# Performance work log

Hardware: AMD Instinct MI355X
Metric: run time of the kernel (lower is better)

Reference implementation:

```python
import jax, jax.numpy as jnp
import numpy as np

# Model hyperparameters (match init_kwargs)
B, REF_P, IN_P, OUT_P = 32, 256, 256, 256
K, KS = 4, 3
RATIO = 0.25
HIDDEN = int(REF_P * RATIO) + 1  # 65, per canonical attention1d
TEMP = 34.0
STRIDE, PAD, DIL, GROUPS = 1, 1, 1, 1
L, L_REF = 4096, 64


def setup_inputs() -> dict:
    key = jax.random.key(0)
    k0, k1, k2, k3, k4 = jax.random.split(key, 5)
    ref = jax.random.normal(k0, (B, REF_P, L_REF), dtype=jnp.float32)
    x = jax.random.normal(k1, (B, IN_P, L), dtype=jnp.float32)
    # attention1d params: fc1 (1x1 conv, no bias), fc2 (1x1 conv, with bias)
    att_w1 = jax.random.normal(k2, (HIDDEN, REF_P), dtype=jnp.float32) * (1.0 / np.sqrt(REF_P))
    att_w2 = jax.random.normal(k3, (K, HIDDEN), dtype=jnp.float32) * (1.0 / np.sqrt(HIDDEN))
    att_b2 = jnp.zeros((K,), dtype=jnp.float32)
    # kaiming-uniform-ish K-bank of conv kernels: [K, out, in/groups, ks]
    fan_in = (IN_P // GROUPS) * KS
    bound = np.sqrt(6.0 / fan_in)
    weight = jax.random.uniform(k4, (K, OUT_P, IN_P // GROUPS, KS), dtype=jnp.float32,
                                minval=-bound, maxval=bound)
    bias = jnp.zeros((K, OUT_P), dtype=jnp.float32)
    return {"ref": ref, "x": x, "att_w1": att_w1, "att_w2": att_w2,
            "att_b2": att_b2, "weight": weight, "bias": bias}


def reference(ref, x, att_w1, att_w2, att_b2, weight, bias):
    b = x.shape[0]
    # attention1d: global avg pool over length, two 1x1 convs, softmax w/ temperature
    pooled = jnp.mean(ref, axis=-1)                       # [B, REF_P]
    h = jax.nn.relu(pooled @ att_w1.T)                    # [B, HIDDEN]
    logits = h @ att_w2.T + att_b2                        # [B, K]
    attn = jax.nn.softmax(logits / TEMP, axis=1)          # [B, K]
    # aggregate per-sample kernel bank
    agg_w = jnp.einsum('bk,koic->boic', attn, weight)     # [B, OUT, IN/g, KS]
    agg_b = attn @ bias                                   # [B, OUT]
    # batched grouped conv1d, exactly as F.conv1d with groups=B*GROUPS
    xr = x.reshape(1, b * IN_P, -1)                       # [1, B*IN, L]
    wr = agg_w.reshape(b * OUT_P, IN_P // GROUPS, KS)     # [B*OUT, IN/g, KS]
    out = jax.lax.conv_general_dilated(
        xr, wr, window_strides=(STRIDE,), padding=[(PAD, PAD)],
        rhs_dilation=(DIL,), dimension_numbers=('NCH', 'OIH', 'NCH'),
        feature_group_count=b * GROUPS)                   # [1, B*OUT, L_out]
    out = out.reshape(b, OUT_P, -1) + agg_b[:, :, None]
    return out
```

## Files before the change

### kernel.cpp

```cpp
#include <hip/hip_runtime.h>
#include <cstdint>
#include <cstddef>

typedef __bf16 bf16;
typedef bf16 bf16x8 __attribute__((ext_vector_type(8)));
typedef float f32x4 __attribute__((ext_vector_type(4)));

typedef __attribute__((address_space(1))) void as1_void;
typedef __attribute__((address_space(3))) void as3_void;

__device__ __forceinline__ void gload16(const void* g, void* l) {
  __builtin_amdgcn_global_load_lds((const as1_void*)g, (as3_void*)l, 16, 0, 0);
}

__global__ __launch_bounds__(256) void attn_kernel(
    const float* __restrict__ ref, const float* __restrict__ w1,
    const float* __restrict__ w2, const float* __restrict__ b2,
    const float* __restrict__ bias, float* __restrict__ attn,
    float* __restrict__ aggb) {
  const int b = blockIdx.x, t = threadIdx.x;
  __shared__ float pooled[256];
  __shared__ float hsh[65];
  __shared__ float ash[4];
  {
    const float* r = ref + ((size_t)b * 256 + t) * 64;
    float s = 0.f;
    #pragma unroll
    for (int l = 0; l < 64; l += 4) {
      float4 v = *(const float4*)(r + l);
      s += v.x + v.y + v.z + v.w;
    }
    pooled[t] = s * (1.0f / 64.0f);
  }
  __syncthreads();
  if (t < 65) {
    const float* w = w1 + t * 256;
    float s = 0.f;
    for (int p = 0; p < 256; ++p) s += pooled[p] * w[p];
    hsh[t] = fmaxf(s, 0.f);
  }
  __syncthreads();
  if (t == 0) {
    float lg[4];
    for (int k = 0; k < 4; ++k) {
      float s = b2[k];
      for (int j = 0; j < 65; ++j) s += hsh[j] * w2[k * 65 + j];
      lg[k] = s * (1.0f / 34.0f);
    }
    float m = fmaxf(fmaxf(lg[0], lg[1]), fmaxf(lg[2], lg[3]));
    float e[4], se = 0.f;
    for (int k = 0; k < 4; ++k) { e[k] = expf(lg[k] - m); se += e[k]; }
    float inv = 1.0f / se;
    for (int k = 0; k < 4; ++k) { float a = e[k] * inv; ash[k] = a; attn[b * 4 + k] = a; }
  }
  __syncthreads();
  {
    float s = 0.f;
    for (int k = 0; k < 4; ++k) s += ash[k] * bias[k * 256 + t];
    aggb[b * 256 + t] = s;
  }
}

__global__ __launch_bounds__(256) void aggw_kernel(
    const float* __restrict__ weight, const float* __restrict__ attn,
    bf16* __restrict__ Wagg) {
  const int o = blockIdx.x, b = blockIdx.y, i = threadIdx.x;
  const float a0 = attn[b * 4 + 0], a1 = attn[b * 4 + 1];
  const float a2 = attn[b * 4 + 2], a3 = attn[b * 4 + 3];
  const size_t ks = (size_t)256 * 256 * 3;
  const float* w = weight + ((size_t)o * 256 + i) * 3;
  bf16* dst = Wagg + ((size_t)(b * 256 + o)) * 768 + i;
  #pragma unroll
  for (int s = 0; s < 3; ++s) {
    float v = a0 * w[s] + a1 * w[ks + s] + a2 * w[2 * ks + s] + a3 * w[3 * ks + s];
    dst[s * 256] = (bf16)v;
  }
}

__global__ __launch_bounds__(256, 3) void conv_kernel(
    const float* __restrict__ x, const bf16* __restrict__ Wagg,
    const float* __restrict__ aggb, float* __restrict__ out) {
  __shared__ bf16 Wl[2][128 * 64];
  __shared__ bf16 Xl[130 * 64];
  const int tid = threadIdx.x;
  const int lane = tid & 63, wid = tid >> 6;
  const int bid = blockIdx.x;
  const int swz = (bid & 7) * 256 + (bid >> 3);
  const int b  = swz >> 6;
  const int ot = (swz >> 5) & 1;
  const int lt = swz & 31;
  const int l0 = lt * 128, o0 = ot * 128;
  const int wm = wid >> 1, wn = wid & 1;
  const float* xb = x + (size_t)b * 256 * 4096;
  const bf16* Wb = Wagg + ((size_t)(b * 256 + o0)) * 768;
  f32x4 acc[4][4] = {};

  auto stage_w = [&](int step, int buf) {
    const int s = step % 3, ib = step / 3;
    const int koff = s * 256 + ib * 64;
    #pragma unroll
    for (int r = 0; r < 4; ++r) {
      int c = r * 256 + tid;
      int row = c >> 3, subg = (c & 7) ^ (row & 7);
      gload16(Wb + (size_t)row * 768 + koff + subg * 8,
              (char*)&Wl[buf][0] + (r * 256 + wid * 64) * 16);
    }
  };

  const int sg = tid >> 5, lc = tid & 31;
  const float* xmain = xb + ((size_t)sg * 8) * 4096 + l0 + lc * 4;
  const int eg = (tid >> 1) & 7;
  const int erow = (tid & 1) ? 129 : 0;
  const int el = (tid & 1) ? (l0 + 128) : (l0 - 1);
  const bool edge_ok = (el >= 0) && (el < 4096);

  float4 xv[8];

  auto load_x = [&](int ib) {
    const float* p = xmain + (size_t)ib * 64 * 4096;
    #pragma unroll
    for (int r = 0; r < 8; ++r)
      xv[r] = *(const float4*)(p + (size_t)r * 4096);
  };
  auto write_x = [&](int ib) {
    char* base = (char*)&Xl[0];
    #pragma unroll
    for (int q = 0; q < 4; ++q) {
      const int row = lc * 4 + 1 + q;
      bf16x8 pk;
      #pragma unroll
      for (int r = 0; r < 8; ++r) pk[r] = (bf16)(((const float*)&xv[r])[q]);
      *(bf16x8*)(base + row * 128 + ((sg ^ (row & 7)) << 4)) = pk;
    }
    if (tid < 16) {
      bf16x8 pe;
      #pragma unroll
      for (int r = 0; r < 8; ++r) {
        float v = edge_ok ? xb[(size_t)(ib * 64 + eg * 8 + r) * 4096 + el] : 0.f;
        pe[r] = (bf16)v;
      }
      *(bf16x8*)(base + erow * 128 + ((eg ^ (erow & 7)) << 4)) = pe;
    }
  };

  load_x(0);
  stage_w(0, 0);
  write_x(0);
  __syncthreads();

  for (int ib = 0; ib < 4; ++ib) {
    if (ib < 3) load_x(ib + 1);
    const char* xbuf = (const char*)&Xl[0];
    #pragma unroll
    for (int s = 0; s < 3; ++s) {
      const int step = ib * 3 + s;
      if (step < 11) stage_w(step + 1, (step + 1) & 1);
      const char* wbuf = (const char*)&Wl[step & 1][0];
      #pragma unroll
      for (int kk = 0; kk < 2; ++kk) {
        const int sub = (lane >> 4) + kk * 4;
        bf16x8 af[4], bfr[4];
        #pragma unroll
        for (int m = 0; m < 4; ++m) {
          int row = wm * 64 + m * 16 + (lane & 15);
          af[m] = *(const bf16x8*)(wbuf + row * 128 + ((sub ^ (row & 7)) << 4));
        }
        #pragma unroll
        for (int n = 0; n < 4; ++n) {
          int row = wn * 64 + n * 16 + (lane & 15) + s;
          bfr[n] = *(const bf16x8*)(xbuf + row * 128 + ((sub ^ (row & 7)) << 4));
        }
        #pragma unroll
        for (int m = 0; m < 4; ++m)
          #pragma unroll
          for (int n = 0; n < 4; ++n)
            acc[m][n] = __builtin_amdgcn_mfma_f32_16x16x32_bf16(af[m], bfr[n], acc[m][n], 0, 0, 0);
      }
      if (step < 11) __syncthreads();
    }
    if (ib < 3) {
      write_x(ib + 1);
      __syncthreads();
    }
  }

  const int b256 = b * 256;
  #pragma unroll
  for (int m = 0; m < 4; ++m) {
    const int ob = o0 + wm * 64 + m * 16 + ((lane >> 4) << 2);
    float bb[4];
    #pragma unroll
    for (int r = 0; r < 4; ++r) bb[r] = aggb[b256 + ob + r];
    #pragma unroll
    for (int n = 0; n < 4; ++n) {
      const int l = l0 + wn * 64 + n * 16 + (lane & 15);
      f32x4 v = acc[m][n];
      #pragma unroll
      for (int r = 0; r < 4; ++r)
        out[((size_t)(b256 + ob + r)) * 4096 + l] = v[r] + bb[r];
    }
  }
}

extern "C" void kernel_launch(void* const* d_in, const int* in_sizes, int n_in,
                              void* d_out, int out_size, void* d_ws, size_t ws_size,
                              hipStream_t stream) {
  const float* ref    = (const float*)d_in[0];
  const float* x      = (const float*)d_in[1];
  const float* w1     = (const float*)d_in[2];
  const float* w2     = (const float*)d_in[3];
  const float* b2     = (const float*)d_in[4];
  const float* weight = (const float*)d_in[5];
  const float* bias   = (const float*)d_in[6];
  float* out = (float*)d_out;
  char* ws = (char*)d_ws;

  const size_t WAGG_BYTES = (size_t)32 * 256 * 768 * 2;
  bf16* Wagg  = (bf16*)ws;
  float* attn = (float*)(ws + WAGG_BYTES);
  float* aggb = (float*)(ws + WAGG_BYTES + 512);

  attn_kernel<<<32, 256, 0, stream>>>(ref, w1, w2, b2, bias, attn, aggb);
  aggw_kernel<<<dim3(256, 32), 256, 0, stream>>>(weight, attn, Wagg);
  conv_kernel<<<2048, 256, 0, stream>>>(x, Wagg, aggb, out);
}
```

Measured before the change: 124.1 us.

## Load weight fragments directly from global memory instead of staging through LDS

Removes the double-buffered LDS staging of the aggregated weight tile (global_load_lds) and its per-step barriers. Each lane now reads its bf16x8 A-fragments straight from global memory, relying on L1/L2 caching since two waves share the same weight rows. LDS usage drops and occupancy may rise now that the launch-bounds minimum is removed. The cost is more global/L2 traffic and exposed load latency inside the MFMA loop, with no prefetch to hide it.

```diff
diff --git a/kernel.cpp b/kernel.cpp
--- a/kernel.cpp
+++ b/kernel.cpp
@@ -5,13 +5,6 @@
 typedef __bf16 bf16;
 typedef bf16 bf16x8 __attribute__((ext_vector_type(8)));
 typedef float f32x4 __attribute__((ext_vector_type(4)));
-
-typedef __attribute__((address_space(1))) void as1_void;
-typedef __attribute__((address_space(3))) void as3_void;
-
-__device__ __forceinline__ void gload16(const void* g, void* l) {
-  __builtin_amdgcn_global_load_lds((const as1_void*)g, (as3_void*)l, 16, 0, 0);
-}
 
 __global__ __launch_bounds__(256) void attn_kernel(
     const float* __restrict__ ref, const float* __restrict__ w1,
@@ -77,10 +70,9 @@
   }
 }
 
-__global__ __launch_bounds__(256, 3) void conv_kernel(
+__global__ __launch_bounds__(256) void conv_kernel(
     const float* __restrict__ x, const bf16* __restrict__ Wagg,
     const float* __restrict__ aggb, float* __restrict__ out) {
-  __shared__ bf16 Wl[2][128 * 64];
   __shared__ bf16 Xl[130 * 64];
   const int tid = threadIdx.x;
   const int lane = tid & 63, wid = tid >> 6;
@@ -92,20 +84,9 @@
   const int l0 = lt * 128, o0 = ot * 128;
   const int wm = wid >> 1, wn = wid & 1;
   const float* xb = x + (size_t)b * 256 * 4096;
-  const bf16* Wb = Wagg + ((size_t)(b * 256 + o0)) * 768;
+  const bf16* wlane = Wagg + ((size_t)(b * 256 + o0 + wm * 64 + (lane & 15))) * 768
+                      + ((lane >> 4) << 3);
   f32x4 acc[4][4] = {};
-
-  auto stage_w = [&](int step, int buf) {
-    const int s = step % 3, ib = step / 3;
-    const int koff = s * 256 + ib * 64;
-    #pragma unroll
-    for (int r = 0; r < 4; ++r) {
-      int c = r * 256 + tid;
-      int row = c >> 3, subg = (c & 7) ^ (row & 7);
-      gload16(Wb + (size_t)row * 768 + koff + subg * 8,
-              (char*)&Wl[buf][0] + (r * 256 + wid * 64) * 16);
-    }
-  };
 
   const int sg = tid >> 5, lc = tid & 31;
   const float* xmain = xb + ((size_t)sg * 8) * 4096 + l0 + lc * 4;
@@ -144,7 +125,6 @@
   };
 
   load_x(0);
-  stage_w(0, 0);
   write_x(0);
   __syncthreads();
 
@@ -153,18 +133,14 @@
     const char* xbuf = (const char*)&Xl[0];
     #pragma unroll
     for (int s = 0; s < 3; ++s) {
-      const int step = ib * 3 + s;
-      if (step < 11) stage_w(step + 1, (step + 1) & 1);
-      const char* wbuf = (const char*)&Wl[step & 1][0];
+      const int kbase = s * 256 + ib * 64;
       #pragma unroll
       for (int kk = 0; kk < 2; ++kk) {
-        const int sub = (lane >> 4) + kk * 4;
         bf16x8 af[4], bfr[4];
         #pragma unroll
-        for (int m = 0; m < 4; ++m) {
-          int row = wm * 64 + m * 16 + (lane & 15);
-          af[m] = *(const bf16x8*)(wbuf + row * 128 + ((sub ^ (row & 7)) << 4));
-        }
+        for (int m = 0; m < 4; ++m)
+          af[m] = *(const bf16x8*)(wlane + (size_t)m * 16 * 768 + kbase + kk * 32);
+        const int sub = (lane >> 4) + kk * 4;
         #pragma unroll
         for (int n = 0; n < 4; ++n) {
           int row = wn * 64 + n * 16 + (lane & 15) + s;
@@ -176,9 +152,9 @@
           for (int n = 0; n < 4; ++n)
             acc[m][n] = __builtin_amdgcn_mfma_f32_16x16x32_bf16(af[m], bfr[n], acc[m][n], 0, 0, 0);
       }
-      if (step < 11) __syncthreads();
     }
     if (ib < 3) {
+      __syncthreads();
       write_x(ib + 1);
       __syncthreads();
     }
```

After: 170.7 us. 1.38x slower.
